# Optimization experiments

Hardware: AMD Instinct MI355X
Metric: run time of the kernel (lower is better)

Reference implementation:

```python
import jax, jax.numpy as jnp
import numpy as np

LN_EPS = 1e-5
IH_IDX = np.array([0, 2, 4, 6])  # layernorm_iih, fih, aih, oih
HH_IDX = np.array([1, 3, 5, 7])  # layernorm_ihh, fhh, ahh, ohh


def _ln(x, g, b):
    # LayerNorm over last dim, matching nn.LayerNorm(hidden_size)
    mu = jnp.mean(x, axis=-1, keepdims=True)
    xc = x - mu
    var = jnp.mean(xc * xc, axis=-1, keepdims=True)
    return g * xc * jax.lax.rsqrt(var + LN_EPS) + b


def setup_inputs() -> dict:
    B, I, H = 4096, 1024, 1024
    key = jax.random.key(0)
    ks = jax.random.split(key, 8)
    stdv = 1.0 / np.sqrt(H)  # reset_parameters: uniform(-stdv, stdv)
    return {
        "x": jax.random.normal(ks[0], (B, I), jnp.float32),
        "h": jax.random.normal(ks[1], (B, H), jnp.float32),
        "c": jax.random.normal(ks[2], (B, H), jnp.float32),
        "w_ih": jax.random.uniform(ks[3], (4 * H, I), jnp.float32, -stdv, stdv),
        "w_hh": jax.random.uniform(ks[4], (4 * H, H), jnp.float32, -stdv, stdv),
        "b_ih": jax.random.uniform(ks[5], (4 * H,), jnp.float32, -stdv, stdv),
        # 9 LayerNorms stacked: [iih, ihh, fih, fhh, aih, ahh, oih, ohh, ct]
        "ln_gamma": 1.0 + 0.1 * jax.random.normal(ks[6], (9, H), jnp.float32),
        "ln_beta": 0.1 * jax.random.normal(ks[7], (9, H), jnp.float32),
        "time": 0,
    }


def reference(x, h, c, w_ih, w_hh, b_ih, ln_gamma, ln_beta, time):
    B = x.shape[0]
    H = w_hh.shape[1]
    # pre-activations, split into the 4 gates (i, f, a, o) along dim 1
    pre_ih = (x @ w_ih.T).reshape(B, 4, H)   # [B,4,H]
    pre_hh = (h @ w_hh.T).reshape(B, 4, H)   # [B,4,H]
    # per-gate LayerNorm on ih and hh contributions, then add bias
    gates = (
        _ln(pre_ih, ln_gamma[IH_IDX], ln_beta[IH_IDX])
        + _ln(pre_hh, ln_gamma[HH_IDX], ln_beta[HH_IDX])
        + b_ih.reshape(4, H)
    )
    i, f, a, o = gates[:, 0], gates[:, 1], gates[:, 2], gates[:, 3]
    c_new = jax.nn.sigmoid(f) * c + jax.nn.sigmoid(i) * jnp.tanh(a)
    h_new = jax.nn.sigmoid(o) * jnp.tanh(_ln(c_new, ln_gamma[8], ln_beta[8]))
    return (h_new, c_new)
```

## Files before the change

### kernel.cpp

```cpp
#include <hip/hip_runtime.h>
#include <hip/hip_bf16.h>
#include <stdint.h>


#define HDIM 1024
#define BATCH 4096
#define NGATE 4096
#define KDIM 1024

typedef __bf16 bf16x8 __attribute__((ext_vector_type(8)));
typedef float f32x4 __attribute__((ext_vector_type(4)));
typedef unsigned short ushort8_t __attribute__((ext_vector_type(8)));

__device__ __forceinline__ unsigned short f2bf(float f) {
  unsigned int u = __builtin_bit_cast(unsigned int, f);
  unsigned int r = (u + 0x7fffu + ((u >> 16) & 1u)) >> 16;
  return (unsigned short)r;
}

__device__ __forceinline__ float bf2f(unsigned short s) {
  unsigned int u = ((unsigned int)s) << 16;
  return __builtin_bit_cast(float, u);
}

__device__ __forceinline__ void gl_lds16(const void* g, void* l) {
  __builtin_amdgcn_global_load_lds(
      (__attribute__((address_space(1))) unsigned int*)g,
      (__attribute__((address_space(3))) unsigned int*)l,
      16, 0, 0);
}

__global__ __launch_bounds__(256) void cast_bf16_kernel(
    const float* __restrict__ x, const float* __restrict__ h,
    const float* __restrict__ wi, const float* __restrict__ wh,
    unsigned short* __restrict__ xb, unsigned short* __restrict__ hb,
    unsigned short* __restrict__ wib, unsigned short* __restrict__ whb) {
  const float* src;
  unsigned short* dst;
  switch (blockIdx.y) {
    case 0: src = x;  dst = xb;  break;
    case 1: src = h;  dst = hb;  break;
    case 2: src = wi; dst = wib; break;
    default: src = wh; dst = whb; break;
  }
  size_t i = ((size_t)blockIdx.x * 256 + threadIdx.x) * 4;
  float4 v = *(const float4*)(src + i);
  ushort4 o;
  o.x = f2bf(v.x); o.y = f2bf(v.y); o.z = f2bf(v.z); o.w = f2bf(v.w);
  *(ushort4*)(dst + i) = o;
}

__global__ __launch_bounds__(256, 4) void gemm_bt_kernel(
    const unsigned short* __restrict__ A0, const unsigned short* __restrict__ B0,
    unsigned short* __restrict__ C0,
    const unsigned short* __restrict__ A1, const unsigned short* __restrict__ B1,
    unsigned short* __restrict__ C1) {
  const unsigned short* A = blockIdx.z ? A1 : A0;
  const unsigned short* B = blockIdx.z ? B1 : B0;
  unsigned short* C = blockIdx.z ? C1 : C0;

  __shared__ alignas(16) unsigned short As[128 * 64];
  __shared__ alignas(16) unsigned short Bs[128 * 64];

  const int tid = threadIdx.x;
  const int wave = tid >> 6;
  const int lane = tid & 63;
  const int bm = blockIdx.x * 128;
  const int bn = blockIdx.y * 128;
  const int wm = (wave >> 1) * 64;
  const int wn = (wave & 1) * 64;

  const int srow = lane >> 3;
  const int scol = (((lane & 7) ^ (lane >> 3)) * 8);

  f32x4 acc[4][4];
#pragma unroll
  for (int i = 0; i < 4; ++i)
#pragma unroll
    for (int j = 0; j < 4; ++j)
#pragma unroll
      for (int r = 0; r < 4; ++r) acc[i][j][r] = 0.0f;

  const int m15 = lane & 15;
  const int quad = lane >> 4;

  for (int k0 = 0; k0 < KDIM; k0 += 64) {
#pragma unroll
    for (int t = 0; t < 4; ++t) {
      int R = wave * 32 + t * 8;
      gl_lds16(A + (size_t)(bm + R + srow) * KDIM + k0 + scol, &As[R * 64]);
      gl_lds16(B + (size_t)(bn + R + srow) * KDIM + k0 + scol, &Bs[R * 64]);
    }
    __syncthreads();

#pragma unroll
    for (int s = 0; s < 2; ++s) {
      bf16x8 af[4], bfr[4];
#pragma unroll
      for (int i = 0; i < 4; ++i) {
        int row = wm + i * 16 + m15;
        af[i] = *(const bf16x8*)&As[row * 64 + (((4 * s + quad) ^ (m15 & 7)) * 8)];
      }
#pragma unroll
      for (int j = 0; j < 4; ++j) {
        int row = wn + j * 16 + m15;
        bfr[j] = *(const bf16x8*)&Bs[row * 64 + (((4 * s + quad) ^ (m15 & 7)) * 8)];
      }
#pragma unroll
      for (int i = 0; i < 4; ++i)
#pragma unroll
        for (int j = 0; j < 4; ++j)
          acc[i][j] = __builtin_amdgcn_mfma_f32_16x16x32_bf16(af[i], bfr[j], acc[i][j], 0, 0, 0);
    }

    __syncthreads();
  }

#pragma unroll
  for (int i = 0; i < 4; ++i)
#pragma unroll
    for (int j = 0; j < 4; ++j)
#pragma unroll
      for (int r = 0; r < 4; ++r) {
        int m = bm + wm + i * 16 + quad * 4 + r;
        int n = bn + wn + j * 16 + m15;
        C[(size_t)m * NGATE + n] = f2bf(acc[i][j][r]);
      }
}

__device__ __forceinline__ float fast_sigmoid(float x) {
  return __builtin_amdgcn_rcpf(1.0f + __expf(-x));
}
__device__ __forceinline__ float fast_tanh(float x) {
  return 1.0f - 2.0f * __builtin_amdgcn_rcpf(__expf(2.0f * x) + 1.0f);
}

__global__ __launch_bounds__(256) void ln_gate_kernel(
    const unsigned short* __restrict__ pih, const unsigned short* __restrict__ phh,
    const float* __restrict__ c, const float* __restrict__ b_ih,
    const float* __restrict__ gamma, const float* __restrict__ beta,
    float* __restrict__ h_out, float* __restrict__ c_out) {
  __shared__ float lds[32];
  const int b = blockIdx.x;
  const int t = threadIdx.x;
  const int wave = t >> 6;
  const int lane = t & 63;
  const float inv_h = 1.0f / 1024.0f;
  const float eps = 1e-5f;

  {
    const size_t rb = (size_t)b * NGATE + wave * HDIM + lane * 16;
    ushort8_t a0 = *(const ushort8_t*)&pih[rb];
    ushort8_t a1 = *(const ushort8_t*)&pih[rb + 8];
    ushort8_t e0 = *(const ushort8_t*)&phh[rb];
    ushort8_t e1 = *(const ushort8_t*)&phh[rb + 8];
    float s0 = 0.f, q0 = 0.f, s1 = 0.f, q1 = 0.f;
#pragma unroll
    for (int r = 0; r < 8; ++r) {
      float va = bf2f(a0[r]), vb = bf2f(a1[r]);
      float ea = bf2f(e0[r]), eb = bf2f(e1[r]);
      s0 += va + vb; q0 += va * va + vb * vb;
      s1 += ea + eb; q1 += ea * ea + eb * eb;
    }
#pragma unroll
    for (int o = 1; o < 64; o <<= 1) {
      s0 += __shfl_xor(s0, o, 64); q0 += __shfl_xor(q0, o, 64);
      s1 += __shfl_xor(s1, o, 64); q1 += __shfl_xor(q1, o, 64);
    }
    if (lane == 0) {
      float mu0 = s0 * inv_h;
      float mu1 = s1 * inv_h;
      lds[wave * 4 + 0] = mu0;
      lds[wave * 4 + 1] = rsqrtf(q0 * inv_h - mu0 * mu0 + eps);
      lds[wave * 4 + 2] = mu1;
      lds[wave * 4 + 3] = rsqrtf(q1 * inv_h - mu1 * mu1 + eps);
    }
  }
  __syncthreads();

  const int j = t * 4;
  float gate[4][4];
#pragma unroll
  for (int g = 0; g < 4; ++g) {
    float mu0 = lds[g * 4 + 0], rs0 = lds[g * 4 + 1];
    float mu1 = lds[g * 4 + 2], rs1 = lds[g * 4 + 3];
    ushort4 a4 = *(const ushort4*)&pih[(size_t)b * NGATE + g * HDIM + j];
    ushort4 e4 = *(const ushort4*)&phh[(size_t)b * NGATE + g * HDIM + j];
    float vih[4] = {bf2f(a4.x), bf2f(a4.y), bf2f(a4.z), bf2f(a4.w)};
    float vhh[4] = {bf2f(e4.x), bf2f(e4.y), bf2f(e4.z), bf2f(e4.w)};
    float4 g0 = *(const float4*)&gamma[(2 * g) * HDIM + j];
    float4 b0 = *(const float4*)&beta[(2 * g) * HDIM + j];
    float4 g1 = *(const float4*)&gamma[(2 * g + 1) * HDIM + j];
    float4 b1 = *(const float4*)&beta[(2 * g + 1) * HDIM + j];
    float4 bb = *(const float4*)&b_ih[g * HDIM + j];
    const float* g0p = &g0.x; const float* b0p = &b0.x;
    const float* g1p = &g1.x; const float* b1p = &b1.x;
    const float* bbp = &bb.x;
#pragma unroll
    for (int r = 0; r < 4; ++r) {
      float gih = g0p[r] * ((vih[r] - mu0) * rs0) + b0p[r];
      float ghh = g1p[r] * ((vhh[r] - mu1) * rs1) + b1p[r];
      gate[g][r] = gih + ghh + bbp[r];
    }
  }

  float4 cv4 = *(const float4*)&c[(size_t)b * HDIM + j];
  const float* cvp = &cv4.x;
  float cn[4], ov[4];
  float s2 = 0.f, q2 = 0.f;
#pragma unroll
  for (int r = 0; r < 4; ++r) {
    float iv = fast_sigmoid(gate[0][r]);
    float fv = fast_sigmoid(gate[1][r]);
    float av = fast_tanh(gate[2][r]);
    ov[r] = fast_sigmoid(gate[3][r]);
    float cvn = fv * cvp[r] + iv * av;
    cn[r] = cvn;
    s2 += cvn; q2 += cvn * cvn;
  }
#pragma unroll
  for (int o = 1; o < 64; o <<= 1) {
    s2 += __shfl_xor(s2, o, 64);
    q2 += __shfl_xor(q2, o, 64);
  }
  __syncthreads();
  if (lane == 0) { lds[16 + wave * 2] = s2; lds[16 + wave * 2 + 1] = q2; }
  __syncthreads();
  s2 = lds[16] + lds[18] + lds[20] + lds[22];
  q2 = lds[17] + lds[19] + lds[21] + lds[23];
  float mu = s2 * inv_h;
  float rs = rsqrtf(q2 * inv_h - mu * mu + eps);

  float4 g8 = *(const float4*)&gamma[8 * HDIM + j];
  float4 b8 = *(const float4*)&beta[8 * HDIM + j];
  const float* g8p = &g8.x; const float* b8p = &b8.x;
  float4 ho, co;
  float* hop = &ho.x; float* cop = &co.x;
#pragma unroll
  for (int r = 0; r < 4; ++r) {
    float ln = g8p[r] * ((cn[r] - mu) * rs) + b8p[r];
    hop[r] = ov[r] * fast_tanh(ln);
    cop[r] = cn[r];
  }
  *(float4*)&h_out[(size_t)b * HDIM + j] = ho;
  *(float4*)&c_out[(size_t)b * HDIM + j] = co;
}

extern "C" void kernel_launch(void* const* d_in, const int* in_sizes, int n_in,
                              void* d_out, int out_size, void* d_ws, size_t ws_size,
                              hipStream_t stream) {
  const float* x     = (const float*)d_in[0];
  const float* h     = (const float*)d_in[1];
  const float* c     = (const float*)d_in[2];
  const float* w_ih  = (const float*)d_in[3];
  const float* w_hh  = (const float*)d_in[4];
  const float* b_ih  = (const float*)d_in[5];
  const float* gamma = (const float*)d_in[6];
  const float* beta  = (const float*)d_in[7];

  char* ws = (char*)d_ws;
  unsigned short* xb  = (unsigned short*)(ws);
  unsigned short* hb  = (unsigned short*)(ws + (size_t)8 * 1024 * 1024);
  unsigned short* wib = (unsigned short*)(ws + (size_t)16 * 1024 * 1024);
  unsigned short* whb = (unsigned short*)(ws + (size_t)24 * 1024 * 1024);
  unsigned short* pih = (unsigned short*)(ws + (size_t)32 * 1024 * 1024);
  unsigned short* phh = (unsigned short*)(ws + (size_t)64 * 1024 * 1024);

  dim3 cgrid(4096, 4, 1);
  cast_bf16_kernel<<<cgrid, 256, 0, stream>>>(x, h, w_ih, w_hh, xb, hb, wib, whb);

  dim3 ggrid(32, 32, 2);
  gemm_bt_kernel<<<ggrid, 256, 0, stream>>>(xb, wib, pih, hb, whb, phh);

  float* h_out = (float*)d_out;
  float* c_out = h_out + (size_t)BATCH * HDIM;
  ln_gate_kernel<<<4096, 256, 0, stream>>>(pih, phh, c, b_ih, gamma, beta, h_out, c_out);
}
```

Before: 236.3 us.

## Rewrite GEMM as 256x256 tile with 8 waves and pipelined LDS prefetch

Replaces the 128x128, 4-wave GEMM with 256x256 tiles computed by 8 waves, keeping the tiles in a four-slot LDS ring (two half-tiles per stage, double-buffered across k). Global-to-LDS loads for the next k-steps are issued between MFMA quarters, with explicit vmcnt waits and raw barriers in place of __syncthreads, plus s_setprio around the MFMA bursts. The aim is to raise arithmetic intensity per LDS byte and hide load latency behind compute. In exchange it uses 128KB of LDS, which may limit occupancy, adds fragile hand-written waitcnt sequencing, and leaves only 512 blocks in the grid.

```diff
diff --git a/kernel.cpp b/kernel.cpp
--- a/kernel.cpp
+++ b/kernel.cpp
@@ -29,6 +29,10 @@
       (__attribute__((address_space(3))) unsigned int*)l,
       16, 0, 0);
 }
+
+#define BAR() asm volatile("s_barrier" ::: "memory")
+#define WAITL() asm volatile("s_waitcnt lgkmcnt(0)" ::: "memory")
+#define WAITV(N) asm volatile("s_waitcnt vmcnt(" #N ")" ::: "memory")
 
 __global__ __launch_bounds__(256) void cast_bf16_kernel(
     const float* __restrict__ x, const float* __restrict__ h,
@@ -50,82 +54,122 @@
   *(ushort4*)(dst + i) = o;
 }
 
-__global__ __launch_bounds__(256, 4) void gemm_bt_kernel(
-    const unsigned short* __restrict__ A0, const unsigned short* __restrict__ B0,
-    unsigned short* __restrict__ C0,
-    const unsigned short* __restrict__ A1, const unsigned short* __restrict__ B1,
-    unsigned short* __restrict__ C1) {
-  const unsigned short* A = blockIdx.z ? A1 : A0;
-  const unsigned short* B = blockIdx.z ? B1 : B0;
-  unsigned short* C = blockIdx.z ? C1 : C0;
-
-  __shared__ alignas(16) unsigned short As[128 * 64];
-  __shared__ alignas(16) unsigned short Bs[128 * 64];
+__global__ __launch_bounds__(512, 2) void gemm_bt_kernel(
+    const unsigned short* __restrict__ A0p, const unsigned short* __restrict__ B0p,
+    unsigned short* __restrict__ C0p,
+    const unsigned short* __restrict__ A1p, const unsigned short* __restrict__ B1p,
+    unsigned short* __restrict__ C1p) {
+  const unsigned short* A = blockIdx.z ? A1p : A0p;
+  const unsigned short* B = blockIdx.z ? B1p : B0p;
+  unsigned short* C = blockIdx.z ? C1p : C0p;
+
+  __shared__ alignas(16) unsigned short As[4 * 128 * 64];
+  __shared__ alignas(16) unsigned short Bs[4 * 128 * 64];
 
   const int tid = threadIdx.x;
   const int wave = tid >> 6;
   const int lane = tid & 63;
-  const int bm = blockIdx.x * 128;
-  const int bn = blockIdx.y * 128;
-  const int wm = (wave >> 1) * 64;
-  const int wn = (wave & 1) * 64;
+  const int wr = wave >> 2;
+  const int wc = wave & 3;
+  const int bm = blockIdx.x * 256;
+  const int bn = blockIdx.y * 256;
 
   const int srow = lane >> 3;
-  const int scol = (((lane & 7) ^ (lane >> 3)) * 8);
-
-  f32x4 acc[4][4];
-#pragma unroll
-  for (int i = 0; i < 4; ++i)
-#pragma unroll
-    for (int j = 0; j < 4; ++j)
-#pragma unroll
-      for (int r = 0; r < 4; ++r) acc[i][j][r] = 0.0f;
-
+  const int scol = ((lane & 7) ^ (lane >> 3)) * 8;
   const int m15 = lane & 15;
   const int quad = lane >> 4;
-
-  for (int k0 = 0; k0 < KDIM; k0 += 64) {
-#pragma unroll
-    for (int t = 0; t < 4; ++t) {
-      int R = wave * 32 + t * 8;
-      gl_lds16(A + (size_t)(bm + R + srow) * KDIM + k0 + scol, &As[R * 64]);
-      gl_lds16(B + (size_t)(bn + R + srow) * KDIM + k0 + scol, &Bs[R * 64]);
-    }
-    __syncthreads();
-
-#pragma unroll
-    for (int s = 0; s < 2; ++s) {
-      bf16x8 af[4], bfr[4];
-#pragma unroll
-      for (int i = 0; i < 4; ++i) {
-        int row = wm + i * 16 + m15;
-        af[i] = *(const bf16x8*)&As[row * 64 + (((4 * s + quad) ^ (m15 & 7)) * 8)];
+  const int sw = m15 & 7;
+
+  f32x4 acc[8][4];
+#pragma unroll
+  for (int i = 0; i < 8; ++i)
+#pragma unroll
+    for (int j = 0; j < 4; ++j)
+#pragma unroll
+      for (int r = 0; r < 4; ++r) acc[i][j][r] = 0.0f;
+
+  auto stage = [&](const unsigned short* __restrict__ G, int grow0, int kk,
+                   unsigned short* slot) {
+    gl_lds16(G + (size_t)(grow0 + wave * 8 + srow) * KDIM + kk + scol,
+             slot + wave * 8 * 64);
+    gl_lds16(G + (size_t)(grow0 + 64 + wave * 8 + srow) * KDIM + kk + scol,
+             slot + (64 + wave * 8) * 64);
+  };
+
+  stage(A, bm,       0,  &As[0]);
+  stage(B, bn,       0,  &Bs[0]);
+  stage(A, bm + 128, 0,  &As[1 * 8192]);
+  stage(B, bn + 128, 0,  &Bs[1 * 8192]);
+  stage(A, bm,       64, &As[2 * 8192]);
+  stage(B, bn,       64, &Bs[2 * 8192]);
+  WAITV(8);
+  BAR();
+
+  for (int t = 0; t < 16; ++t) {
+    const int p2  = (t & 1) * 2;
+    const int n2  = ((t + 1) & 1) * 2;
+    const int kk1 = ((t + 1) & 15) * 64;
+    const int kk2 = ((t + 2) & 15) * 64;
+
+#pragma unroll
+    for (int q = 0; q < 4; ++q) {
+      const int h = q >> 1;
+      const int g = q & 1;
+
+      bf16x8 af[4][2], bfr[2][2];
+      const unsigned short* Abase = &As[(p2 + h) * 8192];
+      const unsigned short* Bbase = &Bs[(p2 + g) * 8192];
+#pragma unroll
+      for (int i2 = 0; i2 < 4; ++i2) {
+        int r = wr * 64 + i2 * 16 + m15;
+#pragma unroll
+        for (int s = 0; s < 2; ++s)
+          af[i2][s] = *(const bf16x8*)&Abase[r * 64 + (((s * 4 + quad) ^ sw) << 3)];
       }
 #pragma unroll
-      for (int j = 0; j < 4; ++j) {
-        int row = wn + j * 16 + m15;
-        bfr[j] = *(const bf16x8*)&Bs[row * 64 + (((4 * s + quad) ^ (m15 & 7)) * 8)];
+      for (int j2 = 0; j2 < 2; ++j2) {
+        int r = wc * 32 + j2 * 16 + m15;
+#pragma unroll
+        for (int s = 0; s < 2; ++s)
+          bfr[j2][s] = *(const bf16x8*)&Bbase[r * 64 + (((s * 4 + quad) ^ sw) << 3)];
       }
-#pragma unroll
-      for (int i = 0; i < 4; ++i)
-#pragma unroll
-        for (int j = 0; j < 4; ++j)
-          acc[i][j] = __builtin_amdgcn_mfma_f32_16x16x32_bf16(af[i], bfr[j], acc[i][j], 0, 0, 0);
-    }
-
-    __syncthreads();
-  }
-
-#pragma unroll
-  for (int i = 0; i < 4; ++i)
-#pragma unroll
-    for (int j = 0; j < 4; ++j)
-#pragma unroll
-      for (int r = 0; r < 4; ++r) {
-        int m = bm + wm + i * 16 + quad * 4 + r;
-        int n = bn + wn + j * 16 + m15;
-        C[(size_t)m * NGATE + n] = f2bf(acc[i][j][r]);
-      }
+
+      if (q == 0)      stage(A, bm + 128, kk1, &As[(n2 + 1) * 8192]);
+      else if (q == 1) stage(B, bn + 128, kk1, &Bs[(n2 + 1) * 8192]);
+      else if (q == 2) stage(A, bm,       kk2, &As[p2 * 8192]);
+      else             stage(B, bn,       kk2, &Bs[p2 * 8192]);
+
+      BAR();
+      WAITL();
+      __builtin_amdgcn_s_setprio(1);
+#pragma unroll
+      for (int i2 = 0; i2 < 4; ++i2)
+#pragma unroll
+        for (int j2 = 0; j2 < 2; ++j2) {
+          acc[h * 4 + i2][g * 2 + j2] = __builtin_amdgcn_mfma_f32_16x16x32_bf16(
+              af[i2][0], bfr[j2][0], acc[h * 4 + i2][g * 2 + j2], 0, 0, 0);
+          acc[h * 4 + i2][g * 2 + j2] = __builtin_amdgcn_mfma_f32_16x16x32_bf16(
+              af[i2][1], bfr[j2][1], acc[h * 4 + i2][g * 2 + j2], 0, 0, 0);
+        }
+      __builtin_amdgcn_s_setprio(0);
+      if (q == 0) WAITV(6);
+      if (q == 3) WAITV(8);
+      BAR();
+    }
+  }
+  WAITV(0);
+
+#pragma unroll
+  for (int i = 0; i < 8; ++i) {
+    int m = bm + (i >> 2) * 128 + wr * 64 + (i & 3) * 16 + quad * 4;
+#pragma unroll
+    for (int j = 0; j < 4; ++j) {
+      int n = bn + (j >> 1) * 128 + wc * 32 + (j & 1) * 16 + m15;
+#pragma unroll
+      for (int rr = 0; rr < 4; ++rr)
+        C[(size_t)(m + rr) * NGATE + n] = f2bf(acc[i][j][rr]);
+    }
+  }
 }
 
 __device__ __forceinline__ float fast_sigmoid(float x) {
@@ -269,8 +313,8 @@
   dim3 cgrid(4096, 4, 1);
   cast_bf16_kernel<<<cgrid, 256, 0, stream>>>(x, h, w_ih, w_hh, xb, hb, wib, whb);
 
-  dim3 ggrid(32, 32, 2);
-  gemm_bt_kernel<<<ggrid, 256, 0, stream>>>(xb, wib, pih, hb, whb, phh);
+  dim3 ggrid(16, 16, 2);
+  gemm_bt_kernel<<<ggrid, 512, 0, stream>>>(xb, wib, pih, hb, whb, phh);
 
   float* h_out = (float*)d_out;
   float* c_out = h_out + (size_t)BATCH * HDIM;
```

Result: slower. 260.7 us (+10.3%).
